# Performance work log

Hardware: AMD Instinct MI355X
Metric: run time of the kernel (lower is better)

The kernel has to match this reference:

```python
import jax, jax.numpy as jnp
import numpy as np

N_NODES = 50000
N_EDGES = 800000
D_IN = 64
D_OUT = 64


def setup_inputs() -> dict:
    key = jax.random.key(0)
    ks = jax.random.split(key, 7)
    features = jax.random.normal(ks[0], (N_NODES, D_IN), dtype=jnp.float32)
    # Linear(in,out,bias=False) weight: (out_features, in_features)
    W = jax.random.normal(ks[1], (D_OUT, D_IN), dtype=jnp.float32) / np.sqrt(D_IN)
    bias = jnp.zeros((D_OUT,), dtype=jnp.float32)
    skip_weight = jnp.ones((D_OUT,), dtype=jnp.float32)
    # sparse normalized adjacency as an edge list with scalar weights
    edge_src = jax.random.randint(ks[2], (N_EDGES,), 0, N_NODES, dtype=jnp.int32)
    edge_dst = jax.random.randint(ks[3], (N_EDGES,), 0, N_NODES, dtype=jnp.int32)
    edge_weight = jax.random.uniform(ks[4], (N_EDGES,), dtype=jnp.float32)
    return {
        "features": features,
        "W": W,
        "bias": bias,
        "skip_weight": skip_weight,
        "edge_weight": edge_weight,
        "edge_src": edge_src,
        "edge_dst": edge_dst,
    }


def reference(features, W, bias, skip_weight, edge_weight, edge_src, edge_dst):
    # Feature transform: x @ W^T  -> (n, out_features)
    h = jnp.einsum("nd,od->no", features, W)
    # Skip term: elementwise scale of transformed features
    skip = h * skip_weight
    # Sparse SpMM: aggregate weighted neighbor messages
    msgs = h[edge_src] * edge_weight[:, None]          # (E, out)
    agg = jax.ops.segment_sum(msgs, edge_dst, num_segments=N_NODES)  # (n, out)
    out = skip + agg + bias
    return jax.nn.selu(out)
```

## Files before the change

kernel.cpp:

```cpp
#include <hip/hip_runtime.h>
#include <math.h>

#define N_NODES 50000
#define N_EDGES 800000
#define D 64
#define NB2 782
#define BCAP2 2048
#define EPB 4096

__device__ __forceinline__ float selu_f(float x) {
    const float scale = 1.0507009873554805f;
    const float alpha = 1.6732632423543772f;
    return x > 0.0f ? scale * x : scale * alpha * expm1f(x);
}

__device__ __forceinline__ unsigned int f2bf(float x) {
    unsigned int u = __float_as_uint(x);
    u += 0x7FFFu + ((u >> 16) & 1u);
    return u >> 16;
}

__device__ __forceinline__ float bf2f(unsigned int b) {
    return __uint_as_float(b << 16);
}

__global__ __launch_bounds__(256) void gemm_kernel(const float* __restrict__ feat,
                                                   const float* __restrict__ W,
                                                   unsigned short* __restrict__ hb,
                                                   int* __restrict__ gcursor) {
    __shared__ float Wt[D][68];
    __shared__ float Sf[64][68];
    const int tid = threadIdx.x;
    const int base = blockIdx.x * 64;

    if (blockIdx.x == 0) {
        for (int i = tid; i < NB2; i += 256) gcursor[i] = 0;
    }

    for (int i = tid; i < D * D; i += 256) {
        int o = i >> 6, d = i & 63;
        Wt[d][o] = W[i];
    }
    for (int i = tid; i < 64 * D; i += 256) {
        int r = i >> 6, c = i & 63;
        int row = base + r;
        Sf[r][c] = (row < N_NODES) ? feat[(size_t)row * D + c] : 0.0f;
    }
    __syncthreads();

    const int wv = tid >> 6;
    const int lane = tid & 63;
    const int r = wv * 16 + (lane >> 2);
    const int cg = lane & 3;
    const int row = base + r;
    if (row >= N_NODES) return;

    float4 a0 = {0, 0, 0, 0}, a1 = {0, 0, 0, 0}, a2 = {0, 0, 0, 0}, a3 = {0, 0, 0, 0};
    const int c0 = cg * 16;
#pragma unroll 4
    for (int k = 0; k < D; ++k) {
        const float f = Sf[r][k];
        const float4 w0 = *(const float4*)&Wt[k][c0 + 0];
        const float4 w1 = *(const float4*)&Wt[k][c0 + 4];
        const float4 w2 = *(const float4*)&Wt[k][c0 + 8];
        const float4 w3 = *(const float4*)&Wt[k][c0 + 12];
        a0.x += f * w0.x; a0.y += f * w0.y; a0.z += f * w0.z; a0.w += f * w0.w;
        a1.x += f * w1.x; a1.y += f * w1.y; a1.z += f * w1.z; a1.w += f * w1.w;
        a2.x += f * w2.x; a2.y += f * w2.y; a2.z += f * w2.z; a2.w += f * w2.w;
        a3.x += f * w3.x; a3.y += f * w3.y; a3.z += f * w3.z; a3.w += f * w3.w;
    }

    const size_t obase = (size_t)row * D + c0;
    uint4 p0, p1;
    p0.x = f2bf(a0.x) | (f2bf(a0.y) << 16);
    p0.y = f2bf(a0.z) | (f2bf(a0.w) << 16);
    p0.z = f2bf(a1.x) | (f2bf(a1.y) << 16);
    p0.w = f2bf(a1.z) | (f2bf(a1.w) << 16);
    p1.x = f2bf(a2.x) | (f2bf(a2.y) << 16);
    p1.y = f2bf(a2.z) | (f2bf(a2.w) << 16);
    p1.z = f2bf(a3.x) | (f2bf(a3.y) << 16);
    p1.w = f2bf(a3.z) | (f2bf(a3.w) << 16);
    ((uint4*)(hb + obase))[0] = p0;
    ((uint4*)(hb + obase))[1] = p1;
}

__global__ __launch_bounds__(1024) void scatter_ms(const int* __restrict__ edst,
                                                   const int* __restrict__ esrc,
                                                   const float* __restrict__ ew,
                                                   int* __restrict__ gcursor,
                                                   int2* __restrict__ pay) {
    __shared__ int hist[NB2];
    __shared__ int lexcl[NB2];
    __shared__ int gbase[NB2];
    __shared__ int waveAgg[16];
    __shared__ int2 stage[EPB];

    const int tid = threadIdx.x;
    const int wid = tid >> 6;
    const int lane = tid & 63;
    const int e0 = blockIdx.x * EPB;
    const int cntb = min(EPB, N_EDGES - e0);

    for (int i = tid; i < NB2; i += 1024) hist[i] = 0;
    __syncthreads();

    int2 rec[4];
    int rb[4];
#pragma unroll
    for (int k = 0; k < 4; ++k) {
        const int idx = k * 1024 + tid;
        rb[k] = -1;
        if (idx < cntb) {
            const int e = e0 + idx;
            const int dst = edst[e];
            const int b = dst >> 6;
            rb[k] = b;
            rec[k] = make_int2((esrc[e] & 0xFFFF) | ((dst & 63) << 16) | (b << 22),
                               __float_as_int(ew[e]));
            atomicAdd(&hist[b], 1);
        }
    }
    __syncthreads();

    const int v = (tid < NB2) ? hist[tid] : 0;
    int incl = v;
#pragma unroll
    for (int off = 1; off < 64; off <<= 1) {
        const int t = __shfl_up(incl, off);
        if (lane >= off) incl += t;
    }
    if (lane == 63) waveAgg[wid] = incl;
    __syncthreads();
    if (wid == 0) {
        const int wv = (lane < 16) ? waveAgg[lane] : 0;
        int wincl = wv;
#pragma unroll
        for (int off = 1; off < 16; off <<= 1) {
            const int t = __shfl_up(wincl, off);
            if (lane >= off) wincl += t;
        }
        if (lane < 16) waveAgg[lane] = wincl - wv;
    }
    __syncthreads();
    if (tid < NB2) {
        const int excl = incl - v + waveAgg[wid];
        lexcl[tid] = excl;
        hist[tid] = excl;
        gbase[tid] = (v > 0) ? atomicAdd(&gcursor[tid], v) : 0;
    }
    __syncthreads();

#pragma unroll
    for (int k = 0; k < 4; ++k) {
        if (rb[k] >= 0) {
            const int p = atomicAdd(&hist[rb[k]], 1);
            stage[p] = rec[k];
        }
    }
    __syncthreads();

    for (int i = tid; i < cntb; i += 1024) {
        const int2 r = stage[i];
        const int b = ((unsigned int)r.x) >> 22;
        const int g = gbase[b] + (i - lexcl[b]);
        if (g < BCAP2) pay[(size_t)b * BCAP2 + g] = r;
    }
}

__global__ __launch_bounds__(512) void csr_sort(const int* __restrict__ gcursor,
                                                int2* __restrict__ pay,
                                                int2* __restrict__ nodeinfo) {
    __shared__ int2 stage[BCAP2];
    __shared__ int cntL[64], curL[64];

    const int b = blockIdx.x;
    const int tid = threadIdx.x;
    const int cnt = min(gcursor[b], BCAP2);
    int2* payb = pay + (size_t)b * BCAP2;

    if (tid < 64) cntL[tid] = 0;
    __syncthreads();

    for (int i = tid; i < cnt; i += 512) {
        const int2 r = payb[i];
        stage[i] = r;
        atomicAdd(&cntL[(r.x >> 16) & 63], 1);
    }
    __syncthreads();

    if (tid < 64) {
        const int v = cntL[tid];
        int incl = v;
#pragma unroll
        for (int off = 1; off < 64; off <<= 1) {
            const int t = __shfl_up(incl, off);
            if (tid >= off) incl += t;
        }
        const int excl = incl - v;
        curL[tid] = excl;
        const int node = (b << 6) + tid;
        if (node < N_NODES) nodeinfo[node] = make_int2(b * BCAP2 + excl, v);
    }
    __syncthreads();

    for (int i = tid; i < cnt; i += 512) {
        const int2 r = stage[i];
        const int p = atomicAdd(&curL[(r.x >> 16) & 63], 1);
        payb[p] = r;
    }
}

__global__ __launch_bounds__(256) void agg_epilogue_kernel(const unsigned short* __restrict__ hb,
                                                           const int2* __restrict__ nodeinfo,
                                                           const int2* __restrict__ pay,
                                                           const float* __restrict__ bias,
                                                           const float* __restrict__ skipw,
                                                           float* __restrict__ out) {
    const int gtid = blockIdx.x * 256 + threadIdx.x;
    const int n = gtid >> 6;
    const int lane = gtid & 63;
    if (n >= N_NODES) return;

    const int half = lane >> 5;
    const int sl = lane & 31;

    const int2 info = nodeinfo[n];
    const int beg = info.x;
    const int deg = info.y;

    float a0x = 0.f, a0y = 0.f, a1x = 0.f, a1y = 0.f;
    float a2x = 0.f, a2y = 0.f, a3x = 0.f, a3y = 0.f;

    for (int i = 0; i < deg; i += 64) {
        const int cnt = min(64, deg - i);
        int2 sw = make_int2(0, 0);
        if (lane < cnt) sw = pay[beg + i + lane];

        int j = 0;
        for (; j + 7 < cnt; j += 8) {
            const int s0 = __shfl(sw.x, j + 0 + half) & 0xFFFF;
            const int s1 = __shfl(sw.x, j + 2 + half) & 0xFFFF;
            const int s2 = __shfl(sw.x, j + 4 + half) & 0xFFFF;
            const int s3 = __shfl(sw.x, j + 6 + half) & 0xFFFF;
            const float w0 = __int_as_float(__shfl(sw.y, j + 0 + half));
            const float w1 = __int_as_float(__shfl(sw.y, j + 2 + half));
            const float w2 = __int_as_float(__shfl(sw.y, j + 4 + half));
            const float w3 = __int_as_float(__shfl(sw.y, j + 6 + half));
            const unsigned int g0 = *(const unsigned int*)(hb + ((size_t)s0 << 6) + sl * 2);
            const unsigned int g1 = *(const unsigned int*)(hb + ((size_t)s1 << 6) + sl * 2);
            const unsigned int g2 = *(const unsigned int*)(hb + ((size_t)s2 << 6) + sl * 2);
            const unsigned int g3 = *(const unsigned int*)(hb + ((size_t)s3 << 6) + sl * 2);
            a0x += bf2f(g0 & 0xFFFF) * w0;  a0y += bf2f(g0 >> 16) * w0;
            a1x += bf2f(g1 & 0xFFFF) * w1;  a1y += bf2f(g1 >> 16) * w1;
            a2x += bf2f(g2 & 0xFFFF) * w2;  a2y += bf2f(g2 >> 16) * w2;
            a3x += bf2f(g3 & 0xFFFF) * w3;  a3y += bf2f(g3 >> 16) * w3;
        }
        for (; j + 1 < cnt; j += 2) {
            const int s = __shfl(sw.x, j + half) & 0xFFFF;
            const float w = __int_as_float(__shfl(sw.y, j + half));
            const unsigned int g = *(const unsigned int*)(hb + ((size_t)s << 6) + sl * 2);
            a0x += bf2f(g & 0xFFFF) * w;  a0y += bf2f(g >> 16) * w;
        }
        if (j < cnt) {
            const int s = __shfl(sw.x, j) & 0xFFFF;
            const float w = __int_as_float(__shfl(sw.y, j));
            const unsigned int g = *(const unsigned int*)(hb + ((size_t)s << 6) + sl * 2);
            const float m = (half == 0) ? 1.0f : 0.0f;
            a1x += bf2f(g & 0xFFFF) * w * m;  a1y += bf2f(g >> 16) * w * m;
        }
    }

    float sx = (a0x + a1x) + (a2x + a3x);
    float sy = (a0y + a1y) + (a2y + a3y);
    sx += __shfl_xor(sx, 32);
    sy += __shfl_xor(sy, 32);

    const unsigned int hn = *(const unsigned int*)(hb + ((size_t)n << 6) + sl * 2);
    const float2 kv = ((const float2*)skipw)[sl];
    const float2 bv = ((const float2*)bias)[sl];
    if (half == 0) {
        float2 o;
        o.x = selu_f(bf2f(hn & 0xFFFF) * kv.x + bv.x + sx);
        o.y = selu_f(bf2f(hn >> 16) * kv.y + bv.y + sy);
        ((float2*)(out + ((size_t)n << 6)))[sl] = o;
    }
}

extern "C" void kernel_launch(void* const* d_in, const int* in_sizes, int n_in,
                              void* d_out, int out_size, void* d_ws, size_t ws_size,
                              hipStream_t stream) {
    const float* feat  = (const float*)d_in[0];
    const float* W     = (const float*)d_in[1];
    const float* bias  = (const float*)d_in[2];
    const float* skipw = (const float*)d_in[3];
    const float* ew    = (const float*)d_in[4];
    const int*   esrc  = (const int*)d_in[5];
    const int*   edst  = (const int*)d_in[6];
    float* out = (float*)d_out;

    int2*           pay      = (int2*)d_ws;
    unsigned short* hb       = (unsigned short*)(pay + (size_t)NB2 * BCAP2);
    int2*           nodeinfo = (int2*)(hb + (size_t)N_NODES * D);
    int*            gcursor  = (int*)(nodeinfo + N_NODES);

    gemm_kernel<<<(N_NODES + 63) / 64, 256, 0, stream>>>(feat, W, hb, gcursor);

    scatter_ms<<<(N_EDGES + EPB - 1) / EPB, 1024, 0, stream>>>(edst, esrc, ew, gcursor, pay);

    csr_sort<<<NB2, 512, 0, stream>>>(gcursor, pay, nodeinfo);

    agg_epilogue_kernel<<<(N_NODES * 64 + 255) / 256, 256, 0, stream>>>(
        hb, nodeinfo, pay, bias, skipw, out);
}
```

Baseline: 137.3 us.

## Fuse GEMM and edge scatter into one launch with block-range split

Merges the feature-transform GEMM and the edge-bucketing scatter kernel into a single launch. The first NSCAT blocks do the scatter and the remaining blocks do the GEMM, using 128-row tiles with 1024 threads and a shared dynamic LDS buffer. Cursor zeroing moves to a hipMemsetAsync, since the scatter blocks now run alongside the GEMM blocks and cannot rely on the GEMM zeroing it first. The aim is to remove one kernel boundary and let the two independent stages overlap on the device. In exchange it adds a memset call, and the larger LDS footprint per block may lower occupancy.

```diff
diff --git a/kernel.cpp b/kernel.cpp
--- a/kernel.cpp
+++ b/kernel.cpp
@@ -7,6 +7,9 @@
 #define NB2 782
 #define BCAP2 2048
 #define EPB 4096
+#define NSCAT 196
+#define GROWS 128
+#define NGEMM ((N_NODES + GROWS - 1) / GROWS)
 
 __device__ __forceinline__ float selu_f(float x) {
     const float scale = 1.0507009873554805f;
@@ -24,146 +27,132 @@
     return __uint_as_float(b << 16);
 }
 
-__global__ __launch_bounds__(256) void gemm_kernel(const float* __restrict__ feat,
-                                                   const float* __restrict__ W,
-                                                   unsigned short* __restrict__ hb,
-                                                   int* __restrict__ gcursor) {
-    __shared__ float Wt[D][68];
-    __shared__ float Sf[64][68];
+__global__ __launch_bounds__(1024) void fused_gemm_scatter(const float* __restrict__ feat,
+                                                           const float* __restrict__ W,
+                                                           const int* __restrict__ edst,
+                                                           const int* __restrict__ esrc,
+                                                           const float* __restrict__ ew,
+                                                           unsigned short* __restrict__ hb,
+                                                           int* __restrict__ gcursor,
+                                                           int2* __restrict__ pay) {
+    extern __shared__ char smem[];
     const int tid = threadIdx.x;
-    const int base = blockIdx.x * 64;
-
-    if (blockIdx.x == 0) {
-        for (int i = tid; i < NB2; i += 256) gcursor[i] = 0;
-    }
-
-    for (int i = tid; i < D * D; i += 256) {
-        int o = i >> 6, d = i & 63;
-        Wt[d][o] = W[i];
-    }
-    for (int i = tid; i < 64 * D; i += 256) {
-        int r = i >> 6, c = i & 63;
-        int row = base + r;
-        Sf[r][c] = (row < N_NODES) ? feat[(size_t)row * D + c] : 0.0f;
-    }
-    __syncthreads();
-
-    const int wv = tid >> 6;
-    const int lane = tid & 63;
-    const int r = wv * 16 + (lane >> 2);
-    const int cg = lane & 3;
-    const int row = base + r;
-    if (row >= N_NODES) return;
-
-    float4 a0 = {0, 0, 0, 0}, a1 = {0, 0, 0, 0}, a2 = {0, 0, 0, 0}, a3 = {0, 0, 0, 0};
-    const int c0 = cg * 16;
-#pragma unroll 4
-    for (int k = 0; k < D; ++k) {
-        const float f = Sf[r][k];
-        const float4 w0 = *(const float4*)&Wt[k][c0 + 0];
-        const float4 w1 = *(const float4*)&Wt[k][c0 + 4];
-        const float4 w2 = *(const float4*)&Wt[k][c0 + 8];
-        const float4 w3 = *(const float4*)&Wt[k][c0 + 12];
-        a0.x += f * w0.x; a0.y += f * w0.y; a0.z += f * w0.z; a0.w += f * w0.w;
-        a1.x += f * w1.x; a1.y += f * w1.y; a1.z += f * w1.z; a1.w += f * w1.w;
-        a2.x += f * w2.x; a2.y += f * w2.y; a2.z += f * w2.z; a2.w += f * w2.w;
-        a3.x += f * w3.x; a3.y += f * w3.y; a3.z += f * w3.z; a3.w += f * w3.w;
-    }
-
-    const size_t obase = (size_t)row * D + c0;
-    uint4 p0, p1;
-    p0.x = f2bf(a0.x) | (f2bf(a0.y) << 16);
-    p0.y = f2bf(a0.z) | (f2bf(a0.w) << 16);
-    p0.z = f2bf(a1.x) | (f2bf(a1.y) << 16);
-    p0.w = f2bf(a1.z) | (f2bf(a1.w) << 16);
-    p1.x = f2bf(a2.x) | (f2bf(a2.y) << 16);
-    p1.y = f2bf(a2.z) | (f2bf(a2.w) << 16);
-    p1.z = f2bf(a3.x) | (f2bf(a3.y) << 16);
-    p1.w = f2bf(a3.z) | (f2bf(a3.w) << 16);
-    ((uint4*)(hb + obase))[0] = p0;
-    ((uint4*)(hb + obase))[1] = p1;
-}
-
-__global__ __launch_bounds__(1024) void scatter_ms(const int* __restrict__ edst,
-                                                   const int* __restrict__ esrc,
-                                                   const float* __restrict__ ew,
-                                                   int* __restrict__ gcursor,
-                                                   int2* __restrict__ pay) {
-    __shared__ int hist[NB2];
-    __shared__ int lexcl[NB2];
-    __shared__ int gbase[NB2];
-    __shared__ int waveAgg[16];
-    __shared__ int2 stage[EPB];
-
-    const int tid = threadIdx.x;
-    const int wid = tid >> 6;
-    const int lane = tid & 63;
-    const int e0 = blockIdx.x * EPB;
-    const int cntb = min(EPB, N_EDGES - e0);
-
-    for (int i = tid; i < NB2; i += 1024) hist[i] = 0;
-    __syncthreads();
-
-    int2 rec[4];
-    int rb[4];
-#pragma unroll
-    for (int k = 0; k < 4; ++k) {
-        const int idx = k * 1024 + tid;
-        rb[k] = -1;
-        if (idx < cntb) {
-            const int e = e0 + idx;
-            const int dst = edst[e];
-            const int b = dst >> 6;
-            rb[k] = b;
-            rec[k] = make_int2((esrc[e] & 0xFFFF) | ((dst & 63) << 16) | (b << 22),
-                               __float_as_int(ew[e]));
-            atomicAdd(&hist[b], 1);
-        }
-    }
-    __syncthreads();
-
-    const int v = (tid < NB2) ? hist[tid] : 0;
-    int incl = v;
-#pragma unroll
-    for (int off = 1; off < 64; off <<= 1) {
-        const int t = __shfl_up(incl, off);
-        if (lane >= off) incl += t;
-    }
-    if (lane == 63) waveAgg[wid] = incl;
-    __syncthreads();
-    if (wid == 0) {
-        const int wv = (lane < 16) ? waveAgg[lane] : 0;
-        int wincl = wv;
-#pragma unroll
-        for (int off = 1; off < 16; off <<= 1) {
-            const int t = __shfl_up(wincl, off);
-            if (lane >= off) wincl += t;
-        }
-        if (lane < 16) waveAgg[lane] = wincl - wv;
-    }
-    __syncthreads();
-    if (tid < NB2) {
-        const int excl = incl - v + waveAgg[wid];
-        lexcl[tid] = excl;
-        hist[tid] = excl;
-        gbase[tid] = (v > 0) ? atomicAdd(&gcursor[tid], v) : 0;
-    }
-    __syncthreads();
-
-#pragma unroll
-    for (int k = 0; k < 4; ++k) {
-        if (rb[k] >= 0) {
-            const int p = atomicAdd(&hist[rb[k]], 1);
-            stage[p] = rec[k];
-        }
-    }
-    __syncthreads();
-
-    for (int i = tid; i < cntb; i += 1024) {
-        const int2 r = stage[i];
-        const int b = ((unsigned int)r.x) >> 22;
-        const int g = gbase[b] + (i - lexcl[b]);
-        if (g < BCAP2) pay[(size_t)b * BCAP2 + g] = r;
+
+    if (blockIdx.x < NSCAT) {
+        int* hist    = (int*)smem;
+        int* lexcl   = hist + NB2;
+        int* gbase   = lexcl + NB2;
+        int* waveAgg = gbase + NB2;
+        int2* stage  = (int2*)(waveAgg + 16);
+
+        const int wid = tid >> 6;
+        const int lane = tid & 63;
+        const int e0 = blockIdx.x * EPB;
+        const int cntb = min(EPB, N_EDGES - e0);
+
+        for (int i = tid; i < NB2; i += 1024) hist[i] = 0;
+        __syncthreads();
+
+        int2 rec[4];
+        int rb[4];
+#pragma unroll
+        for (int k = 0; k < 4; ++k) {
+            const int idx = k * 1024 + tid;
+            rb[k] = -1;
+            if (idx < cntb) {
+                const int e = e0 + idx;
+                const int dst = edst[e];
+                const int b = dst >> 6;
+                rb[k] = b;
+                rec[k] = make_int2((esrc[e] & 0xFFFF) | ((dst & 63) << 16) | (b << 22),
+                                   __float_as_int(ew[e]));
+                atomicAdd(&hist[b], 1);
+            }
+        }
+        __syncthreads();
+
+        const int v = (tid < NB2) ? hist[tid] : 0;
+        int incl = v;
+#pragma unroll
+        for (int off = 1; off < 64; off <<= 1) {
+            const int t = __shfl_up(incl, off);
+            if (lane >= off) incl += t;
+        }
+        if (lane == 63) waveAgg[wid] = incl;
+        __syncthreads();
+        if (wid == 0) {
+            const int wv = (lane < 16) ? waveAgg[lane] : 0;
+            int wincl = wv;
+#pragma unroll
+            for (int off = 1; off < 16; off <<= 1) {
+                const int t = __shfl_up(wincl, off);
+                if (lane >= off) wincl += t;
+            }
+            if (lane < 16) waveAgg[lane] = wincl - wv;
+        }
+        __syncthreads();
+        if (tid < NB2) {
+            const int excl = incl - v + waveAgg[wid];
+            lexcl[tid] = excl;
+            hist[tid] = excl;
+            gbase[tid] = (v > 0) ? atomicAdd(&gcursor[tid], v) : 0;
+        }
+        __syncthreads();
+
+#pragma unroll
+        for (int k = 0; k < 4; ++k) {
+            if (rb[k] >= 0) {
+                const int p = atomicAdd(&hist[rb[k]], 1);
+                stage[p] = rec[k];
+            }
+        }
+        __syncthreads();
+
+        for (int i = tid; i < cntb; i += 1024) {
+            const int2 r = stage[i];
+            const int b = ((unsigned int)r.x) >> 22;
+            const int g = gbase[b] + (i - lexcl[b]);
+            if (g < BCAP2) pay[(size_t)b * BCAP2 + g] = r;
+        }
+    } else {
+        float* Wt = (float*)smem;
+        float* Sf = Wt + 64 * 68;
+        const int base = (blockIdx.x - NSCAT) * GROWS;
+
+        for (int i = tid; i < D * D; i += 1024) {
+            int o = i >> 6, d = i & 63;
+            Wt[d * 68 + o] = W[i];
+        }
+        for (int i = tid; i < GROWS * D; i += 1024) {
+            int r = i >> 6, c = i & 63;
+            int row = base + r;
+            Sf[r * 68 + c] = (row < N_NODES) ? feat[(size_t)row * D + c] : 0.0f;
+        }
+        __syncthreads();
+
+        const int r = tid >> 3;
+        const int cg = tid & 7;
+        const int row = base + r;
+        if (row >= N_NODES) return;
+
+        float4 a0 = {0, 0, 0, 0}, a1 = {0, 0, 0, 0};
+        const float* WtC = Wt + cg * 8;
+        const float* SfR = Sf + r * 68;
+#pragma unroll 8
+        for (int k = 0; k < D; ++k) {
+            const float f = SfR[k];
+            const float4 w0 = *(const float4*)(WtC + k * 68);
+            const float4 w1 = *(const float4*)(WtC + k * 68 + 4);
+            a0.x += f * w0.x; a0.y += f * w0.y; a0.z += f * w0.z; a0.w += f * w0.w;
+            a1.x += f * w1.x; a1.y += f * w1.y; a1.z += f * w1.z; a1.w += f * w1.w;
+        }
+
+        uint4 p;
+        p.x = f2bf(a0.x) | (f2bf(a0.y) << 16);
+        p.y = f2bf(a0.z) | (f2bf(a0.w) << 16);
+        p.z = f2bf(a1.x) | (f2bf(a1.y) << 16);
+        p.w = f2bf(a1.z) | (f2bf(a1.w) << 16);
+        *(uint4*)(hb + (size_t)row * D + cg * 8) = p;
     }
 }
 
@@ -303,9 +292,11 @@
     int2*           nodeinfo = (int2*)(hb + (size_t)N_NODES * D);
     int*            gcursor  = (int*)(nodeinfo + N_NODES);
 
-    gemm_kernel<<<(N_NODES + 63) / 64, 256, 0, stream>>>(feat, W, hb, gcursor);
-
-    scatter_ms<<<(N_EDGES + EPB - 1) / EPB, 1024, 0, stream>>>(edst, esrc, ew, gcursor, pay);
+    hipMemsetAsync(gcursor, 0, (size_t)NB2 * sizeof(int), stream);
+
+    const size_t smem = (size_t)(64 * 68 + GROWS * 68) * sizeof(float);
+    fused_gemm_scatter<<<NSCAT + NGEMM, 1024, smem, stream>>>(feat, W, edst, esrc, ew,
+                                                              hb, gcursor, pay);
 
     csr_sort<<<NB2, 512, 0, stream>>>(gcursor, pay, nodeinfo);
 
```

After: 131.0 us. 4.6% less time.
